# Optimization experiments

Hardware: AMD Instinct MI355X
Metric: run time of the kernel (lower is better)

## Reference

```python
import jax, jax.numpy as jnp
import numpy as np

G, N, D, E, F = 1024, 65536, 128, 400000, 4
HID, N_EDGE_TYPES, DIST_TRUNC = 64, 3, 10
EDGE_REP_DIM = 4 * D + F  # 516


def _mlp(x, W1, b1, W2, b2):
    return jnp.dot(jax.nn.relu(jnp.dot(x, W1) + b1), W2) + b2


def setup_inputs() -> dict:
    key = jax.random.key(0)
    ks = jax.random.split(key, 16)
    feats = jax.random.uniform(ks[6], (E, F), dtype=jnp.float32)
    feats = feats.at[:, 0].multiply(12.0)  # distances in [0, 12) to exercise truncation
    s = 0.05
    return {
        'input_molecule_representations': jax.random.normal(ks[0], (G, D), jnp.float32),
        'partial_graph_representations': jax.random.normal(ks[1], (G, D), jnp.float32),
        'node_representations': jax.random.normal(ks[2], (N, D), jnp.float32),
        'focus_node_idx_in_batch': jax.random.randint(ks[3], (G,), 0, N, jnp.int32),
        'node_to_graph_map': jnp.sort(jax.random.randint(ks[4], (N,), 0, G, jnp.int32)),
        'candidate_edge_targets': jax.random.randint(ks[5], (E,), 0, N, jnp.int32),
        'candidate_edge_features': feats,
        'num_graphs_in_batch': G,
        'dist_emb_table': jax.random.normal(ks[7], (DIST_TRUNC, 1), jnp.float32) * s,
        'no_more_edges_rep': jax.random.normal(ks[8], (1, D + F), jnp.float32) * s,
        'scorer_W1': jax.random.normal(ks[9], (EDGE_REP_DIM, HID), jnp.float32) * s,
        'scorer_b1': jnp.zeros((HID,), jnp.float32),
        'scorer_W2': jax.random.normal(ks[10], (HID, 1), jnp.float32) * s,
        'scorer_b2': jnp.zeros((1,), jnp.float32),
        'type_W1': jax.random.normal(ks[11], (EDGE_REP_DIM, HID), jnp.float32) * s,
        'type_b1': jnp.zeros((HID,), jnp.float32),
        'type_W2': jax.random.normal(ks[12], (HID, N_EDGE_TYPES), jnp.float32) * s,
        'type_b2': jnp.zeros((N_EDGE_TYPES,), jnp.float32),
    }


def reference(input_molecule_representations, partial_graph_representations,
              node_representations, focus_node_idx_in_batch, node_to_graph_map,
              candidate_edge_targets, candidate_edge_features, num_graphs_in_batch,
              dist_emb_table, no_more_edges_rep,
              scorer_W1, scorer_b1, scorer_W2, scorer_b2,
              type_W1, type_b1, type_W2, type_b2):
    # focus node rep per graph: [G, D]
    focus_node_reps = node_representations[focus_node_idx_in_batch]
    # [G, 3D]
    graph_and_focus = jnp.concatenate(
        (input_molecule_representations, partial_graph_representations, focus_node_reps), axis=-1)
    # irregular gathers per edge candidate
    valid_target_to_graph = node_to_graph_map[candidate_edge_targets]      # [E]
    gfn_per_edge = graph_and_focus[valid_target_to_graph]                  # [E, 3D]
    target_reps = node_representations[candidate_edge_targets]            # [E, D]
    trunc_dist = jnp.minimum(candidate_edge_features[:, 0],
                             jnp.float32(DIST_TRUNC - 1)).astype(jnp.int32)
    dist_emb = dist_emb_table[trunc_dist]                                  # [E, 1]
    edge_rep = jnp.concatenate(
        (gfn_per_edge, target_reps, dist_emb, candidate_edge_features[:, 1:]), axis=-1)  # [E, 4D+F]
    stop_rep = jnp.concatenate(
        [graph_and_focus, jnp.tile(no_more_edges_rep, (num_graphs_in_batch, 1))], axis=-1)  # [G, 4D+F]
    all_feats = jnp.concatenate([edge_rep, stop_rep], axis=0)              # [E+G, 4D+F]
    edge_candidate_logits = jnp.squeeze(_mlp(all_feats, scorer_W1, scorer_b1, scorer_W2, scorer_b2), axis=-1)
    edge_type_logits = _mlp(edge_rep, type_W1, type_b1, type_W2, type_b2)  # [E, 3]
    return (edge_candidate_logits, edge_type_logits)
```

## Files before the change

### kernel.cpp

```cpp
#include <hip/hip_runtime.h>

using u16    = unsigned short;
using f32x4  = __attribute__((ext_vector_type(4))) float;
using bf16x8 = __attribute__((ext_vector_type(8))) __bf16;

#define E_CNT 400000
#define G_CNT 1024

#define WS_HNR   0u
#define WS_HGF   16777216u
#define WS_WFRAG 17301504u
#define WS_CT    17432576u
#define WS_NMEH  17436672u

__device__ __forceinline__ u16 f2bf(float f) {
  unsigned u = __builtin_bit_cast(unsigned, f);
  return (u16)((u + 0x7fffu + ((u >> 16) & 1u)) >> 16);
}
__device__ __forceinline__ float b2f(u16 v) {
  unsigned u = ((unsigned)v) << 16;
  return __builtin_bit_cast(float, u);
}
__device__ __forceinline__ uint4 pack8(f32x4 a, f32x4 b) {
  uint4 r;
  r.x = (unsigned)f2bf(a[0]) | ((unsigned)f2bf(a[1]) << 16);
  r.y = (unsigned)f2bf(a[2]) | ((unsigned)f2bf(a[3]) << 16);
  r.z = (unsigned)f2bf(b[0]) | ((unsigned)f2bf(b[1]) << 16);
  r.w = (unsigned)f2bf(b[2]) | ((unsigned)f2bf(b[3]) << 16);
  return r;
}
__device__ __forceinline__ float w1c(const float* sW1, const float* tW1, int k, int j) {
  return (j < 64) ? sW1[(size_t)k * 64 + j] : tW1[(size_t)k * 64 + (j - 64)];
}

__global__ __launch_bounds__(256) void k_prep(const float* __restrict__ nme,
                                              const float* __restrict__ sW1,
                                              const float* __restrict__ tW1,
                                              const float* __restrict__ sW2,
                                              const float* __restrict__ tW2,
                                              u16* __restrict__ wfrag,
                                              float* __restrict__ ct,
                                              float* __restrict__ nmeh) {
  int b = blockIdx.x;
  if (b < 256) {
    int idx = b * 256 + threadIdx.x;
    int j = idx & 7, l = (idx >> 3) & 63, fn = (idx >> 9) & 7, c = idx >> 12;
    int col = fn * 16 + (l & 15);
    int k = c * 32 + (l >> 4) * 8 + j;
    wfrag[idx] = f2bf(w1c(sW1, tW1, k, col));
  } else {
    int p = threadIdx.x;
    if (p >= 128) return;
    int q = p >> 3, i = p & 7, j = i * 16 + q;
    ct[0 * 128 + p] = w1c(sW1, tW1, 513, j);
    ct[1 * 128 + p] = w1c(sW1, tW1, 514, j);
    ct[2 * 128 + p] = w1c(sW1, tW1, 515, j);
    ct[3 * 128 + p] = (i < 4) ? sW2[j] : 0.f;
    if (i >= 4) {
      int jj = j - 64;
      ct[4 * 128 + p] = tW2[jj * 3 + 0];
      ct[5 * 128 + p] = tW2[jj * 3 + 1];
      ct[6 * 128 + p] = tW2[jj * 3 + 2];
    } else {
      ct[4 * 128 + p] = 0.f; ct[5 * 128 + p] = 0.f; ct[6 * 128 + p] = 0.f;
    }
    ct[7 * 128 + p] = w1c(sW1, tW1, 512, j);
    float s = 0.f;
    for (int k = 0; k < 132; ++k) s += nme[k] * w1c(sW1, tW1, 384 + k, j);
    nmeh[p] = s;
  }
}

__global__ __launch_bounds__(64) void k_hnr(const float* __restrict__ nr,
                                            const u16* __restrict__ wfrag,
                                            u16* __restrict__ hnr) {
  int l = threadIdx.x, lr = l & 15, lg = l >> 4;
  int row0 = blockIdx.x * 16;
  f32x4 acc[8];
#pragma unroll
  for (int j = 0; j < 8; ++j) acc[j] = (f32x4){0.f, 0.f, 0.f, 0.f};
#pragma unroll
  for (int c2 = 0; c2 < 4; ++c2) {
    const float* ap = nr + (size_t)(row0 + lr) * 128 + c2 * 32 + lg * 8;
    bf16x8 aF = __builtin_bit_cast(bf16x8, pack8(*(const f32x4*)ap, *(const f32x4*)(ap + 4)));
    bf16x8 bF[8];
#pragma unroll
    for (int fn = 0; fn < 8; ++fn)
      bF[fn] = *(const bf16x8*)((const char*)wfrag + (size_t)((12 + c2) * 8 + fn) * 1024 + l * 16);
#pragma unroll
    for (int fn = 0; fn < 8; ++fn)
      acc[fn] = __builtin_amdgcn_mfma_f32_16x16x32_bf16(aF, bF[fn], acc[fn], 0, 0, 0);
  }
#pragma unroll
  for (int rg = 0; rg < 4; ++rg) {
    int m = row0 + lg * 4 + rg;
    uint4 pk;
    pk.x = (unsigned)f2bf(acc[0][rg]) | ((unsigned)f2bf(acc[1][rg]) << 16);
    pk.y = (unsigned)f2bf(acc[2][rg]) | ((unsigned)f2bf(acc[3][rg]) << 16);
    pk.z = (unsigned)f2bf(acc[4][rg]) | ((unsigned)f2bf(acc[5][rg]) << 16);
    pk.w = (unsigned)f2bf(acc[6][rg]) | ((unsigned)f2bf(acc[7][rg]) << 16);
    *(uint4*)(hnr + (size_t)m * 128 + lr * 8) = pk;
  }
}

__global__ __launch_bounds__(64) void k_hgf(const float* __restrict__ imr,
                                            const float* __restrict__ pgr,
                                            const float* __restrict__ nr,
                                            const int* __restrict__ focus,
                                            const u16* __restrict__ wfrag,
                                            const float* __restrict__ sb1,
                                            const float* __restrict__ tb1,
                                            const float* __restrict__ nmeh,
                                            const float* __restrict__ ct,
                                            const float* __restrict__ sb2,
                                            float* __restrict__ hgf,
                                            float* __restrict__ out0) {
  int l = threadIdx.x, lr = l & 15, lg = l >> 4;
  int row0 = blockIdx.x * 16;
  int fo = focus[row0 + lr];
  f32x4 acc[8];
#pragma unroll
  for (int j = 0; j < 8; ++j) acc[j] = (f32x4){0.f, 0.f, 0.f, 0.f};
#pragma unroll
  for (int c2 = 0; c2 < 12; ++c2) {
    const float* ap;
    if (c2 < 4)      ap = imr + (size_t)(row0 + lr) * 128 + c2 * 32;
    else if (c2 < 8) ap = pgr + (size_t)(row0 + lr) * 128 + (c2 - 4) * 32;
    else             ap = nr + (size_t)fo * 128 + (c2 - 8) * 32;
    ap += lg * 8;
    bf16x8 aF = __builtin_bit_cast(bf16x8, pack8(*(const f32x4*)ap, *(const f32x4*)(ap + 4)));
    bf16x8 bF[8];
#pragma unroll
    for (int fn = 0; fn < 8; ++fn)
      bF[fn] = *(const bf16x8*)((const char*)wfrag + (size_t)(c2 * 8 + fn) * 1024 + l * 16);
#pragma unroll
    for (int fn = 0; fn < 8; ++fn)
      acc[fn] = __builtin_amdgcn_mfma_f32_16x16x32_bf16(aF, bF[fn], acc[fn], 0, 0, 0);
  }
  f32x4 sb1v, tb1v;
#pragma unroll
  for (int fn = 0; fn < 4; ++fn) {
    sb1v[fn] = sb1[fn * 16 + lr];
    tb1v[fn] = tb1[fn * 16 + lr];
  }
  f32x4 nmv = *(const f32x4*)(nmeh + lr * 8);
  f32x4 w2v = *(const f32x4*)(ct + 3 * 128 + lr * 8);
  float sb2v = sb2[0];
#pragma unroll
  for (int rg = 0; rg < 4; ++rg) {
    int g = row0 + lg * 4 + rg;
    f32x4 v0, v1;
#pragma unroll
    for (int fn = 0; fn < 4; ++fn) v0[fn] = acc[fn][rg] + sb1v[fn];
#pragma unroll
    for (int fn = 0; fn < 4; ++fn) v1[fn] = acc[fn + 4][rg] + tb1v[fn];
    *(f32x4*)(hgf + (size_t)g * 128 + lr * 8) = v0;
    *(f32x4*)(hgf + (size_t)g * 128 + lr * 8 + 4) = v1;
    float sp = 0.f;
#pragma unroll
    for (int i = 0; i < 4; ++i) sp += fmaxf(v0[i] + nmv[i], 0.f) * w2v[i];
#pragma unroll
    for (int m = 1; m < 16; m <<= 1) sp += __shfl_xor(sp, m, 64);
    if (lr == 0) out0[E_CNT + g] = sp + sb2v;
  }
}

__global__ __launch_bounds__(256) void k_edge(
    const u16* __restrict__ hnr, const float* __restrict__ hgf,
    const float* __restrict__ ct, const int* __restrict__ tgt,
    const int* __restrict__ n2g, const float4* __restrict__ feats,
    const float* __restrict__ dtab, const float* __restrict__ sb2,
    const float* __restrict__ tb2, float* __restrict__ out0,
    float* __restrict__ out1) {
  int tid = threadIdx.x;
  int q = tid & 15;
  int base = blockIdx.x * 64 + (tid >> 4);

  f32x4 wf1a = *(const f32x4*)(ct + 0 * 128 + q * 8), wf1b = *(const f32x4*)(ct + 0 * 128 + q * 8 + 4);
  f32x4 wf2a = *(const f32x4*)(ct + 1 * 128 + q * 8), wf2b = *(const f32x4*)(ct + 1 * 128 + q * 8 + 4);
  f32x4 wf3a = *(const f32x4*)(ct + 2 * 128 + q * 8), wf3b = *(const f32x4*)(ct + 2 * 128 + q * 8 + 4);
  f32x4 w2v  = *(const f32x4*)(ct + 3 * 128 + q * 8);
  f32x4 tw0v = *(const f32x4*)(ct + 4 * 128 + q * 8 + 4);
  f32x4 tw1v = *(const f32x4*)(ct + 5 * 128 + q * 8 + 4);
  f32x4 tw2v = *(const f32x4*)(ct + 6 * 128 + q * 8 + 4);
  f32x4 w5a  = *(const f32x4*)(ct + 7 * 128 + q * 8), w5b = *(const f32x4*)(ct + 7 * 128 + q * 8 + 4);
  float sb2v = sb2[0], tb0 = tb2[0], tb1 = tb2[1], tb2s = tb2[2];

#pragma unroll
  for (int it = 0; it < 2; ++it) {
    int eA = base + it * 32, eB = eA + 16;

    int tA = tgt[eA], tB = tgt[eB];
    int gA = n2g[tA], gB = n2g[tB];
    float4 fA = feats[eA], fB = feats[eB];
    union { uint4 v; u16 s[8]; } hnA, hnB;
    hnA.v = *(const uint4*)(hnr + (size_t)tA * 128 + q * 8);
    hnB.v = *(const uint4*)(hnr + (size_t)tB * 128 + q * 8);
    f32x4 hgA0 = *(const f32x4*)(hgf + (size_t)gA * 128 + q * 8);
    f32x4 hgA1 = *(const f32x4*)(hgf + (size_t)gA * 128 + q * 8 + 4);
    f32x4 hgB0 = *(const f32x4*)(hgf + (size_t)gB * 128 + q * 8);
    f32x4 hgB1 = *(const f32x4*)(hgf + (size_t)gB * 128 + q * 8 + 4);
    float fdA = dtab[(int)fminf(fA.x, 9.f)];
    float fdB = dtab[(int)fminf(fB.x, 9.f)];

    float scA = 0.f, t0A = 0.f, t1A = 0.f, t2A = 0.f;
#pragma unroll
    for (int i = 0; i < 4; ++i) {
      float h = hgA0[i] + b2f(hnA.s[i]) + fdA * w5a[i] + fA.y * wf1a[i] + fA.z * wf2a[i] + fA.w * wf3a[i];
      scA += fmaxf(h, 0.f) * w2v[i];
    }
#pragma unroll
    for (int i = 0; i < 4; ++i) {
      float h = hgA1[i] + b2f(hnA.s[4 + i]) + fdA * w5b[i] + fA.y * wf1b[i] + fA.z * wf2b[i] + fA.w * wf3b[i];
      float r = fmaxf(h, 0.f);
      t0A += r * tw0v[i]; t1A += r * tw1v[i]; t2A += r * tw2v[i];
    }
    float scB = 0.f, t0B = 0.f, t1B = 0.f, t2B = 0.f;
#pragma unroll
    for (int i = 0; i < 4; ++i) {
      float h = hgB0[i] + b2f(hnB.s[i]) + fdB * w5a[i] + fB.y * wf1a[i] + fB.z * wf2a[i] + fB.w * wf3a[i];
      scB += fmaxf(h, 0.f) * w2v[i];
    }
#pragma unroll
    for (int i = 0; i < 4; ++i) {
      float h = hgB1[i] + b2f(hnB.s[4 + i]) + fdB * w5b[i] + fB.y * wf1b[i] + fB.z * wf2b[i] + fB.w * wf3b[i];
      float r = fmaxf(h, 0.f);
      t0B += r * tw0v[i]; t1B += r * tw1v[i]; t2B += r * tw2v[i];
    }

#pragma unroll
    for (int m = 1; m < 16; m <<= 1) {
      scA += __shfl_xor(scA, m, 64); t0A += __shfl_xor(t0A, m, 64);
      t1A += __shfl_xor(t1A, m, 64); t2A += __shfl_xor(t2A, m, 64);
      scB += __shfl_xor(scB, m, 64); t0B += __shfl_xor(t0B, m, 64);
      t1B += __shfl_xor(t1B, m, 64); t2B += __shfl_xor(t2B, m, 64);
    }
    if (q == 0) {
      out0[eA] = scA + sb2v;
      out0[eB] = scB + sb2v;
      float* oA = out1 + (size_t)eA * 3;
      oA[0] = t0A + tb0; oA[1] = t1A + tb1; oA[2] = t2A + tb2s;
      float* oB = out1 + (size_t)eB * 3;
      oB[0] = t0B + tb0; oB[1] = t1B + tb1; oB[2] = t2B + tb2s;
    }
  }
}

extern "C" void kernel_launch(void* const* d_in, const int* in_sizes, int n_in,
                              void* d_out, int out_size, void* d_ws, size_t ws_size,
                              hipStream_t stream) {
  const float* imr   = (const float*)d_in[0];
  const float* pgr   = (const float*)d_in[1];
  const float* nr    = (const float*)d_in[2];
  const int*   focus = (const int*)d_in[3];
  const int*   n2g   = (const int*)d_in[4];
  const int*   tgt   = (const int*)d_in[5];
  const float* feats = (const float*)d_in[6];
  const float* dtab  = (const float*)d_in[8];
  const float* nme   = (const float*)d_in[9];
  const float* sW1   = (const float*)d_in[10];
  const float* sb1   = (const float*)d_in[11];
  const float* sW2   = (const float*)d_in[12];
  const float* sb2   = (const float*)d_in[13];
  const float* tW1   = (const float*)d_in[14];
  const float* tb1   = (const float*)d_in[15];
  const float* tW2   = (const float*)d_in[16];
  const float* tb2   = (const float*)d_in[17];

  char* ws = (char*)d_ws;
  u16*   HNR   = (u16*)(ws + WS_HNR);
  float* HGF   = (float*)(ws + WS_HGF);
  u16*   WFRAG = (u16*)(ws + WS_WFRAG);
  float* CT    = (float*)(ws + WS_CT);
  float* NMEH  = (float*)(ws + WS_NMEH);

  float* out0 = (float*)d_out;
  float* out1 = out0 + (E_CNT + G_CNT);

  k_prep<<<257, 256, 0, stream>>>(nme, sW1, tW1, sW2, tW2, WFRAG, CT, NMEH);
  k_hnr<<<4096, 64, 0, stream>>>(nr, WFRAG, HNR);
  k_hgf<<<64, 64, 0, stream>>>(imr, pgr, nr, focus, WFRAG, sb1, tb1, NMEH, CT, sb2, HGF, out0);
  k_edge<<<6250, 256, 0, stream>>>(HNR, HGF, CT, tgt, n2g, (const float4*)feats,
                                   dtab, sb2, tb2, out0, out1);
}
```

Before: 66.08 us.

## Fold per-graph hidden term into per-node table and vectorize edge outputs

Moves the per-graph hidden contribution (graph+focus part of layer 1 plus bias) into a per-node precomputed bf16 table, so the edge kernel no longer gathers node_to_graph or the fp32 per-graph rows for each edge. Each lane group now handles four contiguous edges, using DPP row reductions instead of shuffles and float4 stores for both outputs. The per-graph term is now rounded to bf16 together with the node term, which slightly changes numerics, and k_hgf must run before the node kernel.

```diff
diff --git a/kernel.cpp b/kernel.cpp
--- a/kernel.cpp
+++ b/kernel.cpp
@@ -7,7 +7,7 @@
 #define E_CNT 400000
 #define G_CNT 1024
 
-#define WS_HNR   0u
+#define WS_HND   0u
 #define WS_HGF   16777216u
 #define WS_WFRAG 17301504u
 #define WS_CT    17432576u
@@ -31,6 +31,18 @@
 }
 __device__ __forceinline__ float w1c(const float* sW1, const float* tW1, int k, int j) {
   return (j < 64) ? sW1[(size_t)k * 64 + j] : tW1[(size_t)k * 64 + (j - 64)];
+}
+__device__ __forceinline__ float dpp_red16(float x) {
+  int v;
+  v = __builtin_amdgcn_update_dpp(0, __builtin_bit_cast(int, x), 0xB1, 0xF, 0xF, false);
+  x += __builtin_bit_cast(float, v);
+  v = __builtin_amdgcn_update_dpp(0, __builtin_bit_cast(int, x), 0x4E, 0xF, 0xF, false);
+  x += __builtin_bit_cast(float, v);
+  v = __builtin_amdgcn_update_dpp(0, __builtin_bit_cast(int, x), 0x141, 0xF, 0xF, false);
+  x += __builtin_bit_cast(float, v);
+  v = __builtin_amdgcn_update_dpp(0, __builtin_bit_cast(int, x), 0x140, 0xF, 0xF, false);
+  x += __builtin_bit_cast(float, v);
+  return x;
 }
 
 __global__ __launch_bounds__(256) void k_prep(const float* __restrict__ nme,
@@ -71,38 +83,6 @@
   }
 }
 
-__global__ __launch_bounds__(64) void k_hnr(const float* __restrict__ nr,
-                                            const u16* __restrict__ wfrag,
-                                            u16* __restrict__ hnr) {
-  int l = threadIdx.x, lr = l & 15, lg = l >> 4;
-  int row0 = blockIdx.x * 16;
-  f32x4 acc[8];
-#pragma unroll
-  for (int j = 0; j < 8; ++j) acc[j] = (f32x4){0.f, 0.f, 0.f, 0.f};
-#pragma unroll
-  for (int c2 = 0; c2 < 4; ++c2) {
-    const float* ap = nr + (size_t)(row0 + lr) * 128 + c2 * 32 + lg * 8;
-    bf16x8 aF = __builtin_bit_cast(bf16x8, pack8(*(const f32x4*)ap, *(const f32x4*)(ap + 4)));
-    bf16x8 bF[8];
-#pragma unroll
-    for (int fn = 0; fn < 8; ++fn)
-      bF[fn] = *(const bf16x8*)((const char*)wfrag + (size_t)((12 + c2) * 8 + fn) * 1024 + l * 16);
-#pragma unroll
-    for (int fn = 0; fn < 8; ++fn)
-      acc[fn] = __builtin_amdgcn_mfma_f32_16x16x32_bf16(aF, bF[fn], acc[fn], 0, 0, 0);
-  }
-#pragma unroll
-  for (int rg = 0; rg < 4; ++rg) {
-    int m = row0 + lg * 4 + rg;
-    uint4 pk;
-    pk.x = (unsigned)f2bf(acc[0][rg]) | ((unsigned)f2bf(acc[1][rg]) << 16);
-    pk.y = (unsigned)f2bf(acc[2][rg]) | ((unsigned)f2bf(acc[3][rg]) << 16);
-    pk.z = (unsigned)f2bf(acc[4][rg]) | ((unsigned)f2bf(acc[5][rg]) << 16);
-    pk.w = (unsigned)f2bf(acc[6][rg]) | ((unsigned)f2bf(acc[7][rg]) << 16);
-    *(uint4*)(hnr + (size_t)m * 128 + lr * 8) = pk;
-  }
-}
-
 __global__ __launch_bounds__(64) void k_hgf(const float* __restrict__ imr,
                                             const float* __restrict__ pgr,
                                             const float* __restrict__ nr,
@@ -165,16 +145,50 @@
   }
 }
 
+__global__ __launch_bounds__(64) void k_hnode(const float* __restrict__ nr,
+                                              const u16* __restrict__ wfrag,
+                                              const int* __restrict__ n2g,
+                                              const float* __restrict__ hgf,
+                                              u16* __restrict__ hnode) {
+  int l = threadIdx.x, lr = l & 15, lg = l >> 4;
+  int row0 = blockIdx.x * 16;
+  f32x4 acc[8];
+#pragma unroll
+  for (int j = 0; j < 8; ++j) acc[j] = (f32x4){0.f, 0.f, 0.f, 0.f};
+#pragma unroll
+  for (int c2 = 0; c2 < 4; ++c2) {
+    const float* ap = nr + (size_t)(row0 + lr) * 128 + c2 * 32 + lg * 8;
+    bf16x8 aF = __builtin_bit_cast(bf16x8, pack8(*(const f32x4*)ap, *(const f32x4*)(ap + 4)));
+    bf16x8 bF[8];
+#pragma unroll
+    for (int fn = 0; fn < 8; ++fn)
+      bF[fn] = *(const bf16x8*)((const char*)wfrag + (size_t)((12 + c2) * 8 + fn) * 1024 + l * 16);
+#pragma unroll
+    for (int fn = 0; fn < 8; ++fn)
+      acc[fn] = __builtin_amdgcn_mfma_f32_16x16x32_bf16(aF, bF[fn], acc[fn], 0, 0, 0);
+  }
+#pragma unroll
+  for (int rg = 0; rg < 4; ++rg) {
+    int m = row0 + lg * 4 + rg;
+    int g = n2g[m];
+    f32x4 v0 = *(const f32x4*)(hgf + (size_t)g * 128 + lr * 8);
+    f32x4 v1 = *(const f32x4*)(hgf + (size_t)g * 128 + lr * 8 + 4);
+    f32x4 s0, s1;
+#pragma unroll
+    for (int i = 0; i < 4; ++i) { s0[i] = acc[i][rg] + v0[i]; s1[i] = acc[i + 4][rg] + v1[i]; }
+    *(uint4*)(hnode + (size_t)m * 128 + lr * 8) = pack8(s0, s1);
+  }
+}
+
 __global__ __launch_bounds__(256) void k_edge(
-    const u16* __restrict__ hnr, const float* __restrict__ hgf,
-    const float* __restrict__ ct, const int* __restrict__ tgt,
-    const int* __restrict__ n2g, const float4* __restrict__ feats,
+    const u16* __restrict__ hnode, const float* __restrict__ ct,
+    const int* __restrict__ tgt, const float4* __restrict__ feats,
     const float* __restrict__ dtab, const float* __restrict__ sb2,
     const float* __restrict__ tb2, float* __restrict__ out0,
     float* __restrict__ out1) {
   int tid = threadIdx.x;
   int q = tid & 15;
-  int base = blockIdx.x * 64 + (tid >> 4);
+  int e0 = blockIdx.x * 64 + (tid >> 4) * 4;
 
   f32x4 wf1a = *(const f32x4*)(ct + 0 * 128 + q * 8), wf1b = *(const f32x4*)(ct + 0 * 128 + q * 8 + 4);
   f32x4 wf2a = *(const f32x4*)(ct + 1 * 128 + q * 8), wf2b = *(const f32x4*)(ct + 1 * 128 + q * 8 + 4);
@@ -186,63 +200,48 @@
   f32x4 w5a  = *(const f32x4*)(ct + 7 * 128 + q * 8), w5b = *(const f32x4*)(ct + 7 * 128 + q * 8 + 4);
   float sb2v = sb2[0], tb0 = tb2[0], tb1 = tb2[1], tb2s = tb2[2];
 
-#pragma unroll
-  for (int it = 0; it < 2; ++it) {
-    int eA = base + it * 32, eB = eA + 16;
-
-    int tA = tgt[eA], tB = tgt[eB];
-    int gA = n2g[tA], gB = n2g[tB];
-    float4 fA = feats[eA], fB = feats[eB];
-    union { uint4 v; u16 s[8]; } hnA, hnB;
-    hnA.v = *(const uint4*)(hnr + (size_t)tA * 128 + q * 8);
-    hnB.v = *(const uint4*)(hnr + (size_t)tB * 128 + q * 8);
-    f32x4 hgA0 = *(const f32x4*)(hgf + (size_t)gA * 128 + q * 8);
-    f32x4 hgA1 = *(const f32x4*)(hgf + (size_t)gA * 128 + q * 8 + 4);
-    f32x4 hgB0 = *(const f32x4*)(hgf + (size_t)gB * 128 + q * 8);
-    f32x4 hgB1 = *(const f32x4*)(hgf + (size_t)gB * 128 + q * 8 + 4);
-    float fdA = dtab[(int)fminf(fA.x, 9.f)];
-    float fdB = dtab[(int)fminf(fB.x, 9.f)];
-
-    float scA = 0.f, t0A = 0.f, t1A = 0.f, t2A = 0.f;
+  int t[4];
+#pragma unroll
+  for (int j = 0; j < 4; ++j) t[j] = tgt[e0 + j];
+  float4 f[4];
+#pragma unroll
+  for (int j = 0; j < 4; ++j) f[j] = feats[e0 + j];
+  union { uint4 v; u16 s[8]; } hn[4];
+#pragma unroll
+  for (int j = 0; j < 4; ++j)
+    hn[j].v = *(const uint4*)(hnode + (size_t)t[j] * 128 + q * 8);
+  float fd[4];
+#pragma unroll
+  for (int j = 0; j < 4; ++j) fd[j] = dtab[(int)fminf(f[j].x, 9.f)];
+
+  float sc[4], t0[4], t1[4], t2[4];
+#pragma unroll
+  for (int j = 0; j < 4; ++j) {
+    float s = 0.f, a0 = 0.f, a1 = 0.f, a2 = 0.f;
 #pragma unroll
     for (int i = 0; i < 4; ++i) {
-      float h = hgA0[i] + b2f(hnA.s[i]) + fdA * w5a[i] + fA.y * wf1a[i] + fA.z * wf2a[i] + fA.w * wf3a[i];
-      scA += fmaxf(h, 0.f) * w2v[i];
+      float h = b2f(hn[j].s[i]) + fd[j] * w5a[i] + f[j].y * wf1a[i] + f[j].z * wf2a[i] + f[j].w * wf3a[i];
+      s += fmaxf(h, 0.f) * w2v[i];
     }
 #pragma unroll
     for (int i = 0; i < 4; ++i) {
-      float h = hgA1[i] + b2f(hnA.s[4 + i]) + fdA * w5b[i] + fA.y * wf1b[i] + fA.z * wf2b[i] + fA.w * wf3b[i];
+      float h = b2f(hn[j].s[4 + i]) + fd[j] * w5b[i] + f[j].y * wf1b[i] + f[j].z * wf2b[i] + f[j].w * wf3b[i];
       float r = fmaxf(h, 0.f);
-      t0A += r * tw0v[i]; t1A += r * tw1v[i]; t2A += r * tw2v[i];
+      a0 += r * tw0v[i]; a1 += r * tw1v[i]; a2 += r * tw2v[i];
     }
-    float scB = 0.f, t0B = 0.f, t1B = 0.f, t2B = 0.f;
-#pragma unroll
-    for (int i = 0; i < 4; ++i) {
-      float h = hgB0[i] + b2f(hnB.s[i]) + fdB * w5a[i] + fB.y * wf1a[i] + fB.z * wf2a[i] + fB.w * wf3a[i];
-      scB += fmaxf(h, 0.f) * w2v[i];
-    }
-#pragma unroll
-    for (int i = 0; i < 4; ++i) {
-      float h = hgB1[i] + b2f(hnB.s[4 + i]) + fdB * w5b[i] + fB.y * wf1b[i] + fB.z * wf2b[i] + fB.w * wf3b[i];
-      float r = fmaxf(h, 0.f);
-      t0B += r * tw0v[i]; t1B += r * tw1v[i]; t2B += r * tw2v[i];
-    }
-
-#pragma unroll
-    for (int m = 1; m < 16; m <<= 1) {
-      scA += __shfl_xor(scA, m, 64); t0A += __shfl_xor(t0A, m, 64);
-      t1A += __shfl_xor(t1A, m, 64); t2A += __shfl_xor(t2A, m, 64);
-      scB += __shfl_xor(scB, m, 64); t0B += __shfl_xor(t0B, m, 64);
-      t1B += __shfl_xor(t1B, m, 64); t2B += __shfl_xor(t2B, m, 64);
-    }
-    if (q == 0) {
-      out0[eA] = scA + sb2v;
-      out0[eB] = scB + sb2v;
-      float* oA = out1 + (size_t)eA * 3;
-      oA[0] = t0A + tb0; oA[1] = t1A + tb1; oA[2] = t2A + tb2s;
-      float* oB = out1 + (size_t)eB * 3;
-      oB[0] = t0B + tb0; oB[1] = t1B + tb1; oB[2] = t2B + tb2s;
-    }
+    sc[j] = s; t0[j] = a0; t1[j] = a1; t2[j] = a2;
+  }
+#pragma unroll
+  for (int j = 0; j < 4; ++j) {
+    sc[j] = dpp_red16(sc[j]); t0[j] = dpp_red16(t0[j]);
+    t1[j] = dpp_red16(t1[j]); t2[j] = dpp_red16(t2[j]);
+  }
+  if (q == 0) {
+    *(float4*)(out0 + e0) = make_float4(sc[0] + sb2v, sc[1] + sb2v, sc[2] + sb2v, sc[3] + sb2v);
+    float* o = out1 + (size_t)e0 * 3;
+    *(float4*)(o + 0) = make_float4(t0[0] + tb0, t1[0] + tb1, t2[0] + tb2s, t0[1] + tb0);
+    *(float4*)(o + 4) = make_float4(t1[1] + tb1, t2[1] + tb2s, t0[2] + tb0, t1[2] + tb1);
+    *(float4*)(o + 8) = make_float4(t2[2] + tb2s, t0[3] + tb0, t1[3] + tb1, t2[3] + tb2s);
   }
 }
 
@@ -268,7 +267,7 @@
   const float* tb2   = (const float*)d_in[17];
 
   char* ws = (char*)d_ws;
-  u16*   HNR   = (u16*)(ws + WS_HNR);
+  u16*   HND   = (u16*)(ws + WS_HND);
   float* HGF   = (float*)(ws + WS_HGF);
   u16*   WFRAG = (u16*)(ws + WS_WFRAG);
   float* CT    = (float*)(ws + WS_CT);
@@ -278,8 +277,8 @@
   float* out1 = out0 + (E_CNT + G_CNT);
 
   k_prep<<<257, 256, 0, stream>>>(nme, sW1, tW1, sW2, tW2, WFRAG, CT, NMEH);
-  k_hnr<<<4096, 64, 0, stream>>>(nr, WFRAG, HNR);
   k_hgf<<<64, 64, 0, stream>>>(imr, pgr, nr, focus, WFRAG, sb1, tb1, NMEH, CT, sb2, HGF, out0);
-  k_edge<<<6250, 256, 0, stream>>>(HNR, HGF, CT, tgt, n2g, (const float4*)feats,
+  k_hnode<<<4096, 64, 0, stream>>>(nr, WFRAG, n2g, HGF, HND);
+  k_edge<<<6250, 256, 0, stream>>>(HND, CT, tgt, (const float4*)feats,
                                    dtab, sb2, tb2, out0, out1);
 }
```

Result: faster. 61.73 us, median of 2 (-6.6%).
